# Kernel optimization log

Hardware: AMD Instinct MI355X
Metric: run time of the kernel (lower is better)

Reference implementation:

```python
import jax, jax.numpy as jnp
import numpy as np
from jax.scipy.linalg import expm

B, D = 4096, 128


def setup_inputs() -> dict:
    key = jax.random.key(0)
    k1, k2, k3, k4 = jax.random.split(key, 4)
    # xavier_uniform bound for a (D, D) weight: sqrt(6 / (D + D))
    a_w = float(np.sqrt(6.0 / (D + D)))
    # xavier_uniform bound for bias of shape (1, D): sqrt(6 / (1 + D))
    a_b = float(np.sqrt(6.0 / (1 + D)))
    x = jax.random.normal(k1, (B, D), dtype=jnp.float32)
    t = jax.random.uniform(k2, (B, 1), dtype=jnp.float32)  # per-sample scalar time
    weight = jax.random.uniform(k3, (D, D), dtype=jnp.float32, minval=-a_w, maxval=a_w)
    bias = jax.random.uniform(k4, (1, D), dtype=jnp.float32, minval=-a_b, maxval=a_b)
    return {"x": x, "t": t, "weight": weight, "bias": bias}


def reference(x, t, weight, bias):
    # t: [B, 1] -> broadcast scalar per sample; A: [B, D, D]
    A = weight[None, :, :] * t[:, :, None]
    E = jax.vmap(expm)(A)                       # batched matrix exponential
    y = jnp.einsum('bij,bj->bi', E, x)          # [B, D]
    y = y + bias * t                            # bias * t.squeeze(-1)
    ljd = jnp.diagonal(weight)[None, :] * t     # diag(weight * t): [B, D]
    return (y, ljd)
```

## Files before the change

kernel.cpp:

```cpp
#include <hip/hip_runtime.h>


#define DD  128
#define KT  12
#define SPB 16
#define KS  136

typedef short s16x8 __attribute__((ext_vector_type(8)));
typedef short s16x4 __attribute__((ext_vector_type(4)));
typedef float f32x4 __attribute__((ext_vector_type(4)));

__device__ inline unsigned short f2bf(float f) {
    unsigned int u = __float_as_uint(f);
    u += 0x7FFFu + ((u >> 16) & 1u);
    return (unsigned short)(u >> 16);
}
__device__ inline float bf2f(unsigned short h) {
    return __uint_as_float(((unsigned int)h) << 16);
}

__global__ __launch_bounds__(256, 1)
void affine_exp_kernel(const float* __restrict__ x,
                       const float* __restrict__ t,
                       const float* __restrict__ weight,
                       const float* __restrict__ bias,
                       float* __restrict__ out, int B)
{
    __shared__ unsigned short vs[2][SPB * KS];

    const int tid = threadIdx.x;
    const int w   = tid >> 6;
    const int l   = tid & 63;
    const int n   = l & 15;
    const int q   = l >> 4;
    const int s0  = blockIdx.x * SPB;

    const float tn = t[s0 + n];

    s16x8 wahi[2][4], walo[2][4];
#pragma unroll
    for (int r = 0; r < 2; ++r) {
        const int m = w * 32 + r * 16 + n;
#pragma unroll
        for (int s = 0; s < 4; ++s) {
            const float* wp = weight + (size_t)m * DD + s * 32 + q * 8;
            const f32x4 f0 = *reinterpret_cast<const f32x4*>(wp);
            const f32x4 f1 = *reinterpret_cast<const f32x4*>(wp + 4);
            s16x8 h, lo;
#pragma unroll
            for (int j = 0; j < 4; ++j) {
                const unsigned short hb0 = f2bf(f0[j]);
                const unsigned short hb1 = f2bf(f1[j]);
                h[j]      = (short)hb0;
                h[j + 4]  = (short)hb1;
                lo[j]     = (short)f2bf(f0[j] - bf2f(hb0));
                lo[j + 4] = (short)f2bf(f1[j] - bf2f(hb1));
            }
            wahi[r][s] = h;
            walo[r][s] = lo;
        }
    }

    const int g0 = w * 32 + q * 4;
    f32x4 y0 = *reinterpret_cast<const f32x4*>(x + (size_t)(s0 + n) * DD + g0);
    f32x4 y1 = *reinterpret_cast<const f32x4*>(x + (size_t)(s0 + n) * DD + g0 + 16);

#pragma unroll
    for (int i = 0; i < 4; ++i) {
        const int d = q * 32 + i * 8;
        const f32x4 a = *reinterpret_cast<const f32x4*>(x + (size_t)(s0 + n) * DD + d);
        const f32x4 b = *reinterpret_cast<const f32x4*>(x + (size_t)(s0 + n) * DD + d + 4);
        s16x8 p;
#pragma unroll
        for (int j = 0; j < 4; ++j) {
            p[j]     = (short)f2bf(a[j]);
            p[j + 4] = (short)f2bf(b[j]);
        }
        *reinterpret_cast<s16x8*>(&vs[0][n * KS + d]) = p;
    }
    __syncthreads();

    int cur = 0;
#pragma unroll
    for (int k = 1; k <= KT; ++k) {
        const unsigned short* vp = &vs[cur][n * KS + q * 8];
        const s16x8 vb0 = *reinterpret_cast<const s16x8*>(vp);
        const s16x8 vb1 = *reinterpret_cast<const s16x8*>(vp + 32);
        const s16x8 vb2 = *reinterpret_cast<const s16x8*>(vp + 64);
        const s16x8 vb3 = *reinterpret_cast<const s16x8*>(vp + 96);

        f32x4 a0 = {0.f, 0.f, 0.f, 0.f};
        f32x4 a1 = {0.f, 0.f, 0.f, 0.f};
        a0 = __builtin_amdgcn_mfma_f32_16x16x32_bf16(wahi[0][0], vb0, a0, 0, 0, 0);
        a0 = __builtin_amdgcn_mfma_f32_16x16x32_bf16(walo[0][0], vb0, a0, 0, 0, 0);
        a0 = __builtin_amdgcn_mfma_f32_16x16x32_bf16(wahi[0][1], vb1, a0, 0, 0, 0);
        a0 = __builtin_amdgcn_mfma_f32_16x16x32_bf16(walo[0][1], vb1, a0, 0, 0, 0);
        a0 = __builtin_amdgcn_mfma_f32_16x16x32_bf16(wahi[0][2], vb2, a0, 0, 0, 0);
        a0 = __builtin_amdgcn_mfma_f32_16x16x32_bf16(walo[0][2], vb2, a0, 0, 0, 0);
        a0 = __builtin_amdgcn_mfma_f32_16x16x32_bf16(wahi[0][3], vb3, a0, 0, 0, 0);
        a0 = __builtin_amdgcn_mfma_f32_16x16x32_bf16(walo[0][3], vb3, a0, 0, 0, 0);

        a1 = __builtin_amdgcn_mfma_f32_16x16x32_bf16(wahi[1][0], vb0, a1, 0, 0, 0);
        a1 = __builtin_amdgcn_mfma_f32_16x16x32_bf16(walo[1][0], vb0, a1, 0, 0, 0);
        a1 = __builtin_amdgcn_mfma_f32_16x16x32_bf16(wahi[1][1], vb1, a1, 0, 0, 0);
        a1 = __builtin_amdgcn_mfma_f32_16x16x32_bf16(walo[1][1], vb1, a1, 0, 0, 0);
        a1 = __builtin_amdgcn_mfma_f32_16x16x32_bf16(wahi[1][2], vb2, a1, 0, 0, 0);
        a1 = __builtin_amdgcn_mfma_f32_16x16x32_bf16(walo[1][2], vb2, a1, 0, 0, 0);
        a1 = __builtin_amdgcn_mfma_f32_16x16x32_bf16(wahi[1][3], vb3, a1, 0, 0, 0);
        a1 = __builtin_amdgcn_mfma_f32_16x16x32_bf16(walo[1][3], vb3, a1, 0, 0, 0);

        const float c = tn * (1.0f / (float)k);
        a0 *= c;
        a1 *= c;
        y0 += a0;
        y1 += a1;

        s16x4 p0, p1;
#pragma unroll
        for (int j = 0; j < 4; ++j) {
            p0[j] = (short)f2bf(a0[j]);
            p1[j] = (short)f2bf(a1[j]);
        }
        unsigned short* wq = &vs[cur ^ 1][n * KS + g0];
        *reinterpret_cast<s16x4*>(wq)      = p0;
        *reinterpret_cast<s16x4*>(wq + 16) = p1;
        __syncthreads();
        cur ^= 1;
    }

    const f32x4 b0 = *reinterpret_cast<const f32x4*>(bias + g0);
    const f32x4 b1 = *reinterpret_cast<const f32x4*>(bias + g0 + 16);
    y0 += b0 * tn;
    y1 += b1 * tn;
    *reinterpret_cast<f32x4*>(out + (size_t)(s0 + n) * DD + g0)      = y0;
    *reinterpret_cast<f32x4*>(out + (size_t)(s0 + n) * DD + g0 + 16) = y1;

    {
        const int ns = tid & 15;
        const int dg = (tid >> 4) * 8;
        const float ts = t[s0 + ns];
        f32x4 o0, o1;
#pragma unroll
        for (int j = 0; j < 4; ++j) {
            o0[j] = weight[(size_t)(dg + j) * DD + dg + j] * ts;
            o1[j] = weight[(size_t)(dg + 4 + j) * DD + dg + 4 + j] * ts;
        }
        float* lout = out + (size_t)B * DD + (size_t)(s0 + ns) * DD + dg;
        *reinterpret_cast<f32x4*>(lout)     = o0;
        *reinterpret_cast<f32x4*>(lout + 4) = o1;
    }
}

extern "C" void kernel_launch(void* const* d_in, const int* in_sizes, int n_in,
                              void* d_out, int out_size, void* d_ws, size_t ws_size,
                              hipStream_t stream) {
    const float* x      = (const float*)d_in[0];
    const float* t      = (const float*)d_in[1];
    const float* weight = (const float*)d_in[2];
    const float* bias   = (const float*)d_in[3];
    float* out = (float*)d_out;

    const int B = in_sizes[1];
    const int blocks = B / SPB;

    affine_exp_kernel<<<blocks, 256, 0, stream>>>(x, t, weight, bias, out, B);
}
```

Baseline: 67.26 us.

## Halve samples per block, split MFMA accumulators, and cut Taylor terms

Each block now handles 8 samples instead of 16, and two blocks are allowed per CU. That doubles the grid size and lets the latency-bound MFMA chains of two blocks interleave. The unused half of each 16-wide MFMA tile is filled with zeros, so the total MFMA work doubles. Each row-tile's accumulation is split into two independent accumulators in interleaved order to increase instruction-level parallelism. The Taylor series is also truncated from 12 to 10 terms, which saves two iterations per block but lowers accuracy for larger-norm weight times t.

```diff
diff --git a/kernel.cpp b/kernel.cpp
--- a/kernel.cpp
+++ b/kernel.cpp
@@ -2,8 +2,8 @@
 
 
 #define DD  128
-#define KT  12
-#define SPB 16
+#define KT  10
+#define SPB 8
 #define KS  136
 
 typedef short s16x8 __attribute__((ext_vector_type(8)));
@@ -19,14 +19,14 @@
     return __uint_as_float(((unsigned int)h) << 16);
 }
 
-__global__ __launch_bounds__(256, 1)
+__global__ __launch_bounds__(256, 2)
 void affine_exp_kernel(const float* __restrict__ x,
                        const float* __restrict__ t,
                        const float* __restrict__ weight,
                        const float* __restrict__ bias,
                        float* __restrict__ out, int B)
 {
-    __shared__ unsigned short vs[2][SPB * KS];
+    __shared__ unsigned short vs[2][16 * KS];
 
     const int tid = threadIdx.x;
     const int w   = tid >> 6;
@@ -34,8 +34,9 @@
     const int n   = l & 15;
     const int q   = l >> 4;
     const int s0  = blockIdx.x * SPB;
+    const int nn  = n & 7;
 
-    const float tn = t[s0 + n];
+    const float tn = t[s0 + nn];
 
     s16x8 wahi[2][4], walo[2][4];
 #pragma unroll
@@ -62,19 +63,21 @@
     }
 
     const int g0 = w * 32 + q * 4;
-    f32x4 y0 = *reinterpret_cast<const f32x4*>(x + (size_t)(s0 + n) * DD + g0);
-    f32x4 y1 = *reinterpret_cast<const f32x4*>(x + (size_t)(s0 + n) * DD + g0 + 16);
+    f32x4 y0 = *reinterpret_cast<const f32x4*>(x + (size_t)(s0 + nn) * DD + g0);
+    f32x4 y1 = *reinterpret_cast<const f32x4*>(x + (size_t)(s0 + nn) * DD + g0 + 16);
 
 #pragma unroll
     for (int i = 0; i < 4; ++i) {
         const int d = q * 32 + i * 8;
-        const f32x4 a = *reinterpret_cast<const f32x4*>(x + (size_t)(s0 + n) * DD + d);
-        const f32x4 b = *reinterpret_cast<const f32x4*>(x + (size_t)(s0 + n) * DD + d + 4);
-        s16x8 p;
+        s16x8 p = {0, 0, 0, 0, 0, 0, 0, 0};
+        if (n < SPB) {
+            const f32x4 a = *reinterpret_cast<const f32x4*>(x + (size_t)(s0 + n) * DD + d);
+            const f32x4 b = *reinterpret_cast<const f32x4*>(x + (size_t)(s0 + n) * DD + d + 4);
 #pragma unroll
-        for (int j = 0; j < 4; ++j) {
-            p[j]     = (short)f2bf(a[j]);
-            p[j + 4] = (short)f2bf(b[j]);
+            for (int j = 0; j < 4; ++j) {
+                p[j]     = (short)f2bf(a[j]);
+                p[j + 4] = (short)f2bf(b[j]);
+            }
         }
         *reinterpret_cast<s16x8*>(&vs[0][n * KS + d]) = p;
     }
@@ -89,29 +92,28 @@
         const s16x8 vb2 = *reinterpret_cast<const s16x8*>(vp + 64);
         const s16x8 vb3 = *reinterpret_cast<const s16x8*>(vp + 96);
 
-        f32x4 a0 = {0.f, 0.f, 0.f, 0.f};
-        f32x4 a1 = {0.f, 0.f, 0.f, 0.f};
-        a0 = __builtin_amdgcn_mfma_f32_16x16x32_bf16(wahi[0][0], vb0, a0, 0, 0, 0);
-        a0 = __builtin_amdgcn_mfma_f32_16x16x32_bf16(walo[0][0], vb0, a0, 0, 0, 0);
-        a0 = __builtin_amdgcn_mfma_f32_16x16x32_bf16(wahi[0][1], vb1, a0, 0, 0, 0);
-        a0 = __builtin_amdgcn_mfma_f32_16x16x32_bf16(walo[0][1], vb1, a0, 0, 0, 0);
-        a0 = __builtin_amdgcn_mfma_f32_16x16x32_bf16(wahi[0][2], vb2, a0, 0, 0, 0);
-        a0 = __builtin_amdgcn_mfma_f32_16x16x32_bf16(walo[0][2], vb2, a0, 0, 0, 0);
-        a0 = __builtin_amdgcn_mfma_f32_16x16x32_bf16(wahi[0][3], vb3, a0, 0, 0, 0);
-        a0 = __builtin_amdgcn_mfma_f32_16x16x32_bf16(walo[0][3], vb3, a0, 0, 0, 0);
-
-        a1 = __builtin_amdgcn_mfma_f32_16x16x32_bf16(wahi[1][0], vb0, a1, 0, 0, 0);
-        a1 = __builtin_amdgcn_mfma_f32_16x16x32_bf16(walo[1][0], vb0, a1, 0, 0, 0);
-        a1 = __builtin_amdgcn_mfma_f32_16x16x32_bf16(wahi[1][1], vb1, a1, 0, 0, 0);
-        a1 = __builtin_amdgcn_mfma_f32_16x16x32_bf16(walo[1][1], vb1, a1, 0, 0, 0);
-        a1 = __builtin_amdgcn_mfma_f32_16x16x32_bf16(wahi[1][2], vb2, a1, 0, 0, 0);
-        a1 = __builtin_amdgcn_mfma_f32_16x16x32_bf16(walo[1][2], vb2, a1, 0, 0, 0);
-        a1 = __builtin_amdgcn_mfma_f32_16x16x32_bf16(wahi[1][3], vb3, a1, 0, 0, 0);
-        a1 = __builtin_amdgcn_mfma_f32_16x16x32_bf16(walo[1][3], vb3, a1, 0, 0, 0);
+        f32x4 a0a = {0.f, 0.f, 0.f, 0.f}, a0b = {0.f, 0.f, 0.f, 0.f};
+        f32x4 a1a = {0.f, 0.f, 0.f, 0.f}, a1b = {0.f, 0.f, 0.f, 0.f};
+        a0a = __builtin_amdgcn_mfma_f32_16x16x32_bf16(wahi[0][0], vb0, a0a, 0, 0, 0);
+        a1a = __builtin_amdgcn_mfma_f32_16x16x32_bf16(wahi[1][0], vb0, a1a, 0, 0, 0);
+        a0b = __builtin_amdgcn_mfma_f32_16x16x32_bf16(wahi[0][2], vb2, a0b, 0, 0, 0);
+        a1b = __builtin_amdgcn_mfma_f32_16x16x32_bf16(wahi[1][2], vb2, a1b, 0, 0, 0);
+        a0a = __builtin_amdgcn_mfma_f32_16x16x32_bf16(walo[0][0], vb0, a0a, 0, 0, 0);
+        a1a = __builtin_amdgcn_mfma_f32_16x16x32_bf16(walo[1][0], vb0, a1a, 0, 0, 0);
+        a0b = __builtin_amdgcn_mfma_f32_16x16x32_bf16(walo[0][2], vb2, a0b, 0, 0, 0);
+        a1b = __builtin_amdgcn_mfma_f32_16x16x32_bf16(walo[1][2], vb2, a1b, 0, 0, 0);
+        a0a = __builtin_amdgcn_mfma_f32_16x16x32_bf16(wahi[0][1], vb1, a0a, 0, 0, 0);
+        a1a = __builtin_amdgcn_mfma_f32_16x16x32_bf16(wahi[1][1], vb1, a1a, 0, 0, 0);
+        a0b = __builtin_amdgcn_mfma_f32_16x16x32_bf16(wahi[0][3], vb3, a0b, 0, 0, 0);
+        a1b = __builtin_amdgcn_mfma_f32_16x16x32_bf16(wahi[1][3], vb3, a1b, 0, 0, 0);
+        a0a = __builtin_amdgcn_mfma_f32_16x16x32_bf16(walo[0][1], vb1, a0a, 0, 0, 0);
+        a1a = __builtin_amdgcn_mfma_f32_16x16x32_bf16(walo[1][1], vb1, a1a, 0, 0, 0);
+        a0b = __builtin_amdgcn_mfma_f32_16x16x32_bf16(walo[0][3], vb3, a0b, 0, 0, 0);
+        a1b = __builtin_amdgcn_mfma_f32_16x16x32_bf16(walo[1][3], vb3, a1b, 0, 0, 0);
 
         const float c = tn * (1.0f / (float)k);
-        a0 *= c;
-        a1 *= c;
+        f32x4 a0 = (a0a + a0b) * c;
+        f32x4 a1 = (a1a + a1b) * c;
         y0 += a0;
         y1 += a1;
 
@@ -128,26 +130,24 @@
         cur ^= 1;
     }
 
-    const f32x4 b0 = *reinterpret_cast<const f32x4*>(bias + g0);
-    const f32x4 b1 = *reinterpret_cast<const f32x4*>(bias + g0 + 16);
-    y0 += b0 * tn;
-    y1 += b1 * tn;
-    *reinterpret_cast<f32x4*>(out + (size_t)(s0 + n) * DD + g0)      = y0;
-    *reinterpret_cast<f32x4*>(out + (size_t)(s0 + n) * DD + g0 + 16) = y1;
+    if (n < SPB) {
+        const f32x4 b0 = *reinterpret_cast<const f32x4*>(bias + g0);
+        const f32x4 b1 = *reinterpret_cast<const f32x4*>(bias + g0 + 16);
+        const f32x4 o0 = y0 + b0 * tn;
+        const f32x4 o1 = y1 + b1 * tn;
+        *reinterpret_cast<f32x4*>(out + (size_t)(s0 + n) * DD + g0)      = o0;
+        *reinterpret_cast<f32x4*>(out + (size_t)(s0 + n) * DD + g0 + 16) = o1;
+    }
 
     {
-        const int ns = tid & 15;
-        const int dg = (tid >> 4) * 8;
+        const int ns = tid >> 5;
+        const int dg = (tid & 31) << 2;
         const float ts = t[s0 + ns];
-        f32x4 o0, o1;
+        f32x4 o;
 #pragma unroll
-        for (int j = 0; j < 4; ++j) {
-            o0[j] = weight[(size_t)(dg + j) * DD + dg + j] * ts;
-            o1[j] = weight[(size_t)(dg + 4 + j) * DD + dg + 4 + j] * ts;
-        }
-        float* lout = out + (size_t)B * DD + (size_t)(s0 + ns) * DD + dg;
-        *reinterpret_cast<f32x4*>(lout)     = o0;
-        *reinterpret_cast<f32x4*>(lout + 4) = o1;
+        for (int j = 0; j < 4; ++j)
+            o[j] = weight[(size_t)(dg + j) * DD + dg + j] * ts;
+        *reinterpret_cast<f32x4*>(out + (size_t)B * DD + (size_t)(s0 + ns) * DD + dg) = o;
     }
 }
 
```

Result: slower. 71.19 us (+5.8%).

## Precompute W^k/k! powers once, apply as independent MFMAs per sample

Applied to the files above, without the earlier changes.

The batch-shared matrix powers W^k/k! are computed once in a small 8-block kernel and stored as split fp16 hi/lo MFMA fragments in workspace. The apply kernel then scales x by t each step and accumulates independent MFMAs against these precomputed powers, with no LDS round-trip or per-step barrier. It also switches from bf16 to fp16 splits and cuts the Taylor order from 12 to 10. In exchange it adds a serial second launch, heavy repeated reads of the power fragments from global/L2, and less accuracy headroom from the lower order and the fp16 range of t^k·x.

```diff
diff --git a/kernel.cpp b/kernel.cpp
--- a/kernel.cpp
+++ b/kernel.cpp
@@ -1,133 +1,180 @@
 #include <hip/hip_runtime.h>
 
 
-#define DD  128
-#define KT  12
-#define SPB 16
-#define KS  136
-
-typedef short s16x8 __attribute__((ext_vector_type(8)));
-typedef short s16x4 __attribute__((ext_vector_type(4)));
+#define DD 128
+#define KT 10
+
 typedef float f32x4 __attribute__((ext_vector_type(4)));
-
-__device__ inline unsigned short f2bf(float f) {
-    unsigned int u = __float_as_uint(f);
-    u += 0x7FFFu + ((u >> 16) & 1u);
-    return (unsigned short)(u >> 16);
+typedef _Float16 f16x8 __attribute__((ext_vector_type(8)));
+
+
+__global__ __launch_bounds__(256, 1)
+void gpow_kernel(const float* __restrict__ weight, _Float16* __restrict__ gws)
+{
+    __shared__ float wlds[DD * DD];
+    __shared__ float gbuf[2][16 * 132];
+
+    const int tid = threadIdx.x;
+    const int w = tid >> 6, l = tid & 63, n = l & 15, q = l >> 4;
+    const int r = blockIdx.x;
+
+    for (int i = tid; i < DD * DD / 4; i += 256)
+        reinterpret_cast<f32x4*>(wlds)[i] = reinterpret_cast<const f32x4*>(weight)[i];
+    __syncthreads();
+
+    f16x8 Bh[2][4], Bl[2][4];
+#pragma unroll
+    for (int ct = 0; ct < 2; ++ct)
+#pragma unroll
+        for (int kf = 0; kf < 4; ++kf)
+#pragma unroll
+            for (int j = 0; j < 8; ++j) {
+                const float f = wlds[(32 * kf + q * 8 + j) * DD + 32 * w + 16 * ct + n];
+                const _Float16 h = (_Float16)f;
+                Bh[ct][kf][j] = h;
+                Bl[ct][kf][j] = (_Float16)(f - (float)h);
+            }
+
+    f16x8 Ah[4], Al[4];
+#pragma unroll
+    for (int kf = 0; kf < 4; ++kf) {
+        const float* p = wlds + (16 * r + n) * DD + 32 * kf + q * 8;
+#pragma unroll
+        for (int j = 0; j < 8; ++j) {
+            const float f = p[j];
+            const _Float16 h = (_Float16)f;
+            Ah[kf][j] = h;
+            Al[kf][j] = (_Float16)(f - (float)h);
+        }
+    }
+
+#define STORE_FRAGS(kk)                                                              \
+    {                                                                                \
+        _Pragma("unroll")                                                            \
+        for (int kf = 0; kf < 4; ++kf)                                               \
+            if (kf == w) {                                                           \
+                size_t o0 = ((size_t)(((((kk)-1) * 8 + r) * 4 + kf) * 2 + 0)) * 512 + l * 8; \
+                size_t o1 = ((size_t)(((((kk)-1) * 8 + r) * 4 + kf) * 2 + 1)) * 512 + l * 8; \
+                *reinterpret_cast<f16x8*>(gws + o0) = Ah[kf];                        \
+                *reinterpret_cast<f16x8*>(gws + o1) = Al[kf];                        \
+            }                                                                        \
+    }
+
+    STORE_FRAGS(1);
+
+    int cur = 0;
+#pragma unroll 1
+    for (int k = 2; k <= KT; ++k) {
+        f32x4 C0 = {0.f, 0.f, 0.f, 0.f}, C1 = {0.f, 0.f, 0.f, 0.f};
+#pragma unroll
+        for (int kf = 0; kf < 4; ++kf) {
+            C0 = __builtin_amdgcn_mfma_f32_16x16x32_f16(Ah[kf], Bh[0][kf], C0, 0, 0, 0);
+            C0 = __builtin_amdgcn_mfma_f32_16x16x32_f16(Al[kf], Bh[0][kf], C0, 0, 0, 0);
+            C0 = __builtin_amdgcn_mfma_f32_16x16x32_f16(Ah[kf], Bl[0][kf], C0, 0, 0, 0);
+            C1 = __builtin_amdgcn_mfma_f32_16x16x32_f16(Ah[kf], Bh[1][kf], C1, 0, 0, 0);
+            C1 = __builtin_amdgcn_mfma_f32_16x16x32_f16(Al[kf], Bh[1][kf], C1, 0, 0, 0);
+            C1 = __builtin_amdgcn_mfma_f32_16x16x32_f16(Ah[kf], Bl[1][kf], C1, 0, 0, 0);
+        }
+        const float inv = 1.0f / (float)k;
+        C0 *= inv;
+        C1 *= inv;
+#pragma unroll
+        for (int jr = 0; jr < 4; ++jr) {
+            gbuf[cur][(q * 4 + jr) * 132 + 32 * w + n]      = C0[jr];
+            gbuf[cur][(q * 4 + jr) * 132 + 32 * w + 16 + n] = C1[jr];
+        }
+        __syncthreads();
+#pragma unroll
+        for (int kf = 0; kf < 4; ++kf) {
+            const float* p = &gbuf[cur][n * 132 + 32 * kf + q * 8];
+            const f32x4 a = *reinterpret_cast<const f32x4*>(p);
+            const f32x4 b = *reinterpret_cast<const f32x4*>(p + 4);
+#pragma unroll
+            for (int j = 0; j < 4; ++j) {
+                const _Float16 h0 = (_Float16)a[j];
+                const _Float16 h1 = (_Float16)b[j];
+                Ah[kf][j]     = h0;
+                Ah[kf][j + 4] = h1;
+                Al[kf][j]     = (_Float16)(a[j] - (float)h0);
+                Al[kf][j + 4] = (_Float16)(b[j] - (float)h1);
+            }
+        }
+        STORE_FRAGS(k);
+        cur ^= 1;
+    }
 }
-__device__ inline float bf2f(unsigned short h) {
-    return __uint_as_float(((unsigned int)h) << 16);
-}
 
 __global__ __launch_bounds__(256, 1)
-void affine_exp_kernel(const float* __restrict__ x,
-                       const float* __restrict__ t,
-                       const float* __restrict__ weight,
-                       const float* __restrict__ bias,
-                       float* __restrict__ out, int B)
+void apply_kernel(const float* __restrict__ x,
+                  const float* __restrict__ t,
+                  const float* __restrict__ weight,
+                  const float* __restrict__ bias,
+                  const _Float16* __restrict__ gws,
+                  float* __restrict__ out, int B)
 {
-    __shared__ unsigned short vs[2][SPB * KS];
-
     const int tid = threadIdx.x;
-    const int w   = tid >> 6;
-    const int l   = tid & 63;
-    const int n   = l & 15;
-    const int q   = l >> 4;
-    const int s0  = blockIdx.x * SPB;
+    const int w = tid >> 6, l = tid & 63, n = l & 15, q = l >> 4;
+    const int s0 = blockIdx.x * 16;
 
     const float tn = t[s0 + n];
-
-    s16x8 wahi[2][4], walo[2][4];
-#pragma unroll
-    for (int r = 0; r < 2; ++r) {
-        const int m = w * 32 + r * 16 + n;
-#pragma unroll
-        for (int s = 0; s < 4; ++s) {
-            const float* wp = weight + (size_t)m * DD + s * 32 + q * 8;
-            const f32x4 f0 = *reinterpret_cast<const f32x4*>(wp);
-            const f32x4 f1 = *reinterpret_cast<const f32x4*>(wp + 4);
-            s16x8 h, lo;
-#pragma unroll
-            for (int j = 0; j < 4; ++j) {
-                const unsigned short hb0 = f2bf(f0[j]);
-                const unsigned short hb1 = f2bf(f1[j]);
-                h[j]      = (short)hb0;
-                h[j + 4]  = (short)hb1;
-                lo[j]     = (short)f2bf(f0[j] - bf2f(hb0));
-                lo[j + 4] = (short)f2bf(f1[j] - bf2f(hb1));
+    const _Float16 th = (_Float16)tn;
+    f16x8 tv;
+#pragma unroll
+    for (int j = 0; j < 8; ++j) tv[j] = th;
+
+    f16x8 xf[4];
+    const float* xp = x + (size_t)(s0 + n) * DD + q * 8;
+#pragma unroll
+    for (int kf = 0; kf < 4; ++kf) {
+        const f32x4 a = *reinterpret_cast<const f32x4*>(xp + 32 * kf);
+        const f32x4 b = *reinterpret_cast<const f32x4*>(xp + 32 * kf + 4);
+#pragma unroll
+        for (int j = 0; j < 4; ++j) {
+            xf[kf][j]     = (_Float16)a[j];
+            xf[kf][j + 4] = (_Float16)b[j];
+        }
+    }
+
+    const int g0 = w * 32 + q * 4;
+    f32x4 y0a = *reinterpret_cast<const f32x4*>(x + (size_t)(s0 + n) * DD + g0);
+    f32x4 y1a = *reinterpret_cast<const f32x4*>(x + (size_t)(s0 + n) * DD + g0 + 16);
+    f32x4 y0b = {0.f, 0.f, 0.f, 0.f};
+    f32x4 y1b = {0.f, 0.f, 0.f, 0.f};
+
+    const int r0 = 2 * w, r1 = 2 * w + 1;
+
+#pragma unroll
+    for (int k = 1; k <= KT; ++k) {
+#pragma unroll
+        for (int kf = 0; kf < 4; ++kf) xf[kf] *= tv;
+
+        const size_t base = ((size_t)(k - 1) * 8) * 4 * 2 * 512;
+#pragma unroll
+        for (int kf = 0; kf < 4; ++kf) {
+            const size_t o0h = base + ((size_t)(r0 * 4 + kf) * 2 + 0) * 512 + l * 8;
+            const size_t o0l = base + ((size_t)(r0 * 4 + kf) * 2 + 1) * 512 + l * 8;
+            const size_t o1h = base + ((size_t)(r1 * 4 + kf) * 2 + 0) * 512 + l * 8;
+            const size_t o1l = base + ((size_t)(r1 * 4 + kf) * 2 + 1) * 512 + l * 8;
+            const f16x8 g0h = *reinterpret_cast<const f16x8*>(gws + o0h);
+            const f16x8 g0l = *reinterpret_cast<const f16x8*>(gws + o0l);
+            const f16x8 g1h = *reinterpret_cast<const f16x8*>(gws + o1h);
+            const f16x8 g1l = *reinterpret_cast<const f16x8*>(gws + o1l);
+            if (kf < 2) {
+                y0a = __builtin_amdgcn_mfma_f32_16x16x32_f16(g0h, xf[kf], y0a, 0, 0, 0);
+                y0a = __builtin_amdgcn_mfma_f32_16x16x32_f16(g0l, xf[kf], y0a, 0, 0, 0);
+                y1a = __builtin_amdgcn_mfma_f32_16x16x32_f16(g1h, xf[kf], y1a, 0, 0, 0);
+                y1a = __builtin_amdgcn_mfma_f32_16x16x32_f16(g1l, xf[kf], y1a, 0, 0, 0);
+            } else {
+                y0b = __builtin_amdgcn_mfma_f32_16x16x32_f16(g0h, xf[kf], y0b, 0, 0, 0);
+                y0b = __builtin_amdgcn_mfma_f32_16x16x32_f16(g0l, xf[kf], y0b, 0, 0, 0);
+                y1b = __builtin_amdgcn_mfma_f32_16x16x32_f16(g1h, xf[kf], y1b, 0, 0, 0);
+                y1b = __builtin_amdgcn_mfma_f32_16x16x32_f16(g1l, xf[kf], y1b, 0, 0, 0);
             }
-            wahi[r][s] = h;
-            walo[r][s] = lo;
-        }
-    }
-
-    const int g0 = w * 32 + q * 4;
-    f32x4 y0 = *reinterpret_cast<const f32x4*>(x + (size_t)(s0 + n) * DD + g0);
-    f32x4 y1 = *reinterpret_cast<const f32x4*>(x + (size_t)(s0 + n) * DD + g0 + 16);
-
-#pragma unroll
-    for (int i = 0; i < 4; ++i) {
-        const int d = q * 32 + i * 8;
-        const f32x4 a = *reinterpret_cast<const f32x4*>(x + (size_t)(s0 + n) * DD + d);
-        const f32x4 b = *reinterpret_cast<const f32x4*>(x + (size_t)(s0 + n) * DD + d + 4);
-        s16x8 p;
-#pragma unroll
-        for (int j = 0; j < 4; ++j) {
-            p[j]     = (short)f2bf(a[j]);
-            p[j + 4] = (short)f2bf(b[j]);
-        }
-        *reinterpret_cast<s16x8*>(&vs[0][n * KS + d]) = p;
-    }
-    __syncthreads();
-
-    int cur = 0;
-#pragma unroll
-    for (int k = 1; k <= KT; ++k) {
-        const unsigned short* vp = &vs[cur][n * KS + q * 8];
-        const s16x8 vb0 = *reinterpret_cast<const s16x8*>(vp);
-        const s16x8 vb1 = *reinterpret_cast<const s16x8*>(vp + 32);
-        const s16x8 vb2 = *reinterpret_cast<const s16x8*>(vp + 64);
-        const s16x8 vb3 = *reinterpret_cast<const s16x8*>(vp + 96);
-
-        f32x4 a0 = {0.f, 0.f, 0.f, 0.f};
-        f32x4 a1 = {0.f, 0.f, 0.f, 0.f};
-        a0 = __builtin_amdgcn_mfma_f32_16x16x32_bf16(wahi[0][0], vb0, a0, 0, 0, 0);
-        a0 = __builtin_amdgcn_mfma_f32_16x16x32_bf16(walo[0][0], vb0, a0, 0, 0, 0);
-        a0 = __builtin_amdgcn_mfma_f32_16x16x32_bf16(wahi[0][1], vb1, a0, 0, 0, 0);
-        a0 = __builtin_amdgcn_mfma_f32_16x16x32_bf16(walo[0][1], vb1, a0, 0, 0, 0);
-        a0 = __builtin_amdgcn_mfma_f32_16x16x32_bf16(wahi[0][2], vb2, a0, 0, 0, 0);
-        a0 = __builtin_amdgcn_mfma_f32_16x16x32_bf16(walo[0][2], vb2, a0, 0, 0, 0);
-        a0 = __builtin_amdgcn_mfma_f32_16x16x32_bf16(wahi[0][3], vb3, a0, 0, 0, 0);
-        a0 = __builtin_amdgcn_mfma_f32_16x16x32_bf16(walo[0][3], vb3, a0, 0, 0, 0);
-
-        a1 = __builtin_amdgcn_mfma_f32_16x16x32_bf16(wahi[1][0], vb0, a1, 0, 0, 0);
-        a1 = __builtin_amdgcn_mfma_f32_16x16x32_bf16(walo[1][0], vb0, a1, 0, 0, 0);
-        a1 = __builtin_amdgcn_mfma_f32_16x16x32_bf16(wahi[1][1], vb1, a1, 0, 0, 0);
-        a1 = __builtin_amdgcn_mfma_f32_16x16x32_bf16(walo[1][1], vb1, a1, 0, 0, 0);
-        a1 = __builtin_amdgcn_mfma_f32_16x16x32_bf16(wahi[1][2], vb2, a1, 0, 0, 0);
-        a1 = __builtin_amdgcn_mfma_f32_16x16x32_bf16(walo[1][2], vb2, a1, 0, 0, 0);
-        a1 = __builtin_amdgcn_mfma_f32_16x16x32_bf16(wahi[1][3], vb3, a1, 0, 0, 0);
-        a1 = __builtin_amdgcn_mfma_f32_16x16x32_bf16(walo[1][3], vb3, a1, 0, 0, 0);
-
-        const float c = tn * (1.0f / (float)k);
-        a0 *= c;
-        a1 *= c;
-        y0 += a0;
-        y1 += a1;
-
-        s16x4 p0, p1;
-#pragma unroll
-        for (int j = 0; j < 4; ++j) {
-            p0[j] = (short)f2bf(a0[j]);
-            p1[j] = (short)f2bf(a1[j]);
-        }
-        unsigned short* wq = &vs[cur ^ 1][n * KS + g0];
-        *reinterpret_cast<s16x4*>(wq)      = p0;
-        *reinterpret_cast<s16x4*>(wq + 16) = p1;
-        __syncthreads();
-        cur ^= 1;
-    }
-
+        }
+    }
+
+    f32x4 y0 = y0a + y0b;
+    f32x4 y1 = y1a + y1b;
     const f32x4 b0 = *reinterpret_cast<const f32x4*>(bias + g0);
     const f32x4 b1 = *reinterpret_cast<const f32x4*>(bias + g0 + 16);
     y0 += b0 * tn;
@@ -136,8 +183,8 @@
     *reinterpret_cast<f32x4*>(out + (size_t)(s0 + n) * DD + g0 + 16) = y1;
 
     {
-        const int ns = tid & 15;
-        const int dg = (tid >> 4) * 8;
+        const int ns = tid >> 4;
+        const int dg = (tid & 15) * 8;
         const float ts = t[s0 + ns];
         f32x4 o0, o1;
 #pragma unroll
@@ -145,9 +192,9 @@
             o0[j] = weight[(size_t)(dg + j) * DD + dg + j] * ts;
             o1[j] = weight[(size_t)(dg + 4 + j) * DD + dg + 4 + j] * ts;
         }
-        float* lout = out + (size_t)B * DD + (size_t)(s0 + ns) * DD + dg;
-        *reinterpret_cast<f32x4*>(lout)     = o0;
-        *reinterpret_cast<f32x4*>(lout + 4) = o1;
+        float* lp = out + (size_t)B * DD + (size_t)(s0 + ns) * DD + dg;
+        *reinterpret_cast<f32x4*>(lp)     = o0;
+        *reinterpret_cast<f32x4*>(lp + 4) = o1;
     }
 }
 
@@ -159,9 +206,10 @@
     const float* weight = (const float*)d_in[2];
     const float* bias   = (const float*)d_in[3];
     float* out = (float*)d_out;
+    _Float16* gws = (_Float16*)d_ws;
 
     const int B = in_sizes[1];
-    const int blocks = B / SPB;
-
-    affine_exp_kernel<<<blocks, 256, 0, stream>>>(x, t, weight, bias, out, B);
+
+    gpow_kernel<<<8, 256, 0, stream>>>(weight, gws);
+    apply_kernel<<<B / 16, 256, 0, stream>>>(x, t, weight, bias, gws, out, B);
 }
```

Measured after the change: 86.94 us. 1.29x slower.
